# Performance work log

Measured on AMD Instinct MI355X. Metric: run time of the kernel, lower is better.

The kernel has to match this reference:

```python
import jax, jax.numpy as jnp
import numpy as np

STEP = 5
ALPHA = 0.01
D = 1024
BN_EPS = 1e-5
L2_EPS = 1e-12


def setup_inputs() -> dict:
    key = jax.random.key(0)
    k1, k2 = jax.random.split(key, 2)
    B = 16
    x = jax.random.normal(k1, (B * STEP, D), dtype=jnp.float32)
    W = jax.random.normal(k2, (D, D), dtype=jnp.float32) * 0.02
    b = jnp.zeros((D,), jnp.float32)
    gamma = jnp.ones((D,), jnp.float32)
    beta = jnp.zeros((D,), jnp.float32)
    return {"x": x, "W": W, "b": b, "gamma": gamma, "beta": beta}


def reference(x, W, b, gamma, beta):
    BS = x.shape[0]          # B * STEP
    B = BS // STEP
    x_seq = x.reshape(B, STEP, D)

    def step_fn(h, xt):
        # xt: [B, D]; Hebbian fast-weight update
        # hebb = alpha * (k v^T - k^2 * h)
        hebb = ALPHA * (xt[:, :, None] * xt[:, None, :] - (xt ** 2)[:, :, None] * h)
        h = h + hebb
        return h, h

    h0 = jnp.zeros((B, D, D), x.dtype)
    _, mems = jax.lax.scan(step_fn, h0, jnp.swapaxes(x_seq, 0, 1))  # [STEP, B, D, D]
    # torch.cat(memory_total, dim=0) -> step-major stacking
    mem = mems.reshape(BS, D, D)

    # batched mat-vec readout; x here is batch-major (faithful to original mismatch)
    q = jnp.einsum('nij,nj->ni', mem, x)  # [BS, D]

    y = q @ W.T + b
    # BatchNorm1d in training mode: batch statistics, biased variance
    mu = y.mean(axis=0)
    var = y.var(axis=0)
    yhat = (y - mu) / jnp.sqrt(var + BN_EPS)
    out = jax.nn.relu(yhat * gamma + beta)
    # F.normalize: L2 over dim=1 with eps clamp
    norm = jnp.linalg.norm(out, axis=1, keepdims=True)
    return out / jnp.maximum(norm, L2_EPS)
```

## Files before the change

kernel.cpp:

```cpp
#include <hip/hip_runtime.h>
#include <math.h>

#define D_DIM   1024
#define BS      80
#define STEPS   5
#define ALPHA   0.01f
#define BN_EPS  1e-5f
#define L2_EPS  1e-12f

#define K2_NN   10
#define NG      8
#define A_BLOCKS 512

__global__ __launch_bounds__(256, 2) void kA(const float* __restrict__ x,
                                             const float* __restrict__ W,
                                             const float* __restrict__ bvec,
                                             float* __restrict__ y,
                                             float* __restrict__ psum,
                                             float* __restrict__ psq) {
    const int tid  = threadIdx.x;
    const int lane = tid & 63;
    const int wid  = tid >> 6;
    const int bid  = blockIdx.x;
    const int wave = bid * 4 + wid;
    const int jg   = wave & 255;
    const int j0   = jg * 4;
    const int ng   = bid >> 6;
    const int n0   = ng * K2_NN;

    __shared__ float qs[K2_NN][D_DIM];

    const float4* __restrict__ x4 = (const float4*)x;
    const float4* __restrict__ W4 = (const float4*)W;

    float4 w[4][4];
#pragma unroll
    for (int jj = 0; jj < 4; ++jj)
#pragma unroll
        for (int m = 0; m < 4; ++m)
            w[jj][m] = W4[(size_t)(j0 + jj) * 256 + lane + 64 * m];
    const float4 b4 = ((const float4*)bvec)[jg];

    for (int r = wid; r < K2_NN; r += 4) {
        const int n  = n0 + r;
        const int t  = n >> 4;
        const int bb = n & 15;

        float4 v[4];
#pragma unroll
        for (int m = 0; m < 4; ++m)
            v[m] = x4[(size_t)n * 256 + lane + 64 * m];

        float4 k[STEPS][4];
        float p[STEPS];
#pragma unroll
        for (int s = 0; s < STEPS; ++s) {
            if (s <= t) {
#pragma unroll
                for (int m = 0; m < 4; ++m)
                    k[s][m] = x4[(size_t)(bb * STEPS + s) * 256 + lane + 64 * m];
                float d = 0.f;
#pragma unroll
                for (int m = 0; m < 4; ++m)
                    d += k[s][m].x * v[m].x + k[s][m].y * v[m].y
                       + k[s][m].z * v[m].z + k[s][m].w * v[m].w;
                p[s] = d;
            } else {
                p[s] = 0.f;
            }
        }
#pragma unroll
        for (int off = 32; off; off >>= 1) {
#pragma unroll
            for (int s = 0; s < STEPS; ++s) p[s] += __shfl_xor(p[s], off, 64);
        }

        float4 acc[4];
#pragma unroll
        for (int m = 0; m < 4; ++m) acc[m] = make_float4(0.f, 0.f, 0.f, 0.f);
#pragma unroll
        for (int s = 0; s < STEPS; ++s) {
            if (s <= t) {
#pragma unroll
                for (int m = 0; m < 4; ++m) {
                    acc[m].x = acc[m].x * (1.f - ALPHA * k[s][m].x * k[s][m].x) + p[s] * k[s][m].x;
                    acc[m].y = acc[m].y * (1.f - ALPHA * k[s][m].y * k[s][m].y) + p[s] * k[s][m].y;
                    acc[m].z = acc[m].z * (1.f - ALPHA * k[s][m].z * k[s][m].z) + p[s] * k[s][m].z;
                    acc[m].w = acc[m].w * (1.f - ALPHA * k[s][m].w * k[s][m].w) + p[s] * k[s][m].w;
                }
            }
        }
#pragma unroll
        for (int m = 0; m < 4; ++m) {
            acc[m].x *= ALPHA; acc[m].y *= ALPHA; acc[m].z *= ALPHA; acc[m].w *= ALPHA;
            ((float4*)qs[r])[lane + 64 * m] = acc[m];
        }
    }
    __syncthreads();

    float csum[4] = {0.f, 0.f, 0.f, 0.f};
    float csq [4] = {0.f, 0.f, 0.f, 0.f};

#pragma unroll 2
    for (int nn = 0; nn < K2_NN; ++nn) {
        const int n = n0 + nn;
        float4 qv[4];
#pragma unroll
        for (int m = 0; m < 4; ++m)
            qv[m] = ((const float4*)qs[nn])[lane + 64 * m];

        float s[4] = {0.f, 0.f, 0.f, 0.f};
#pragma unroll
        for (int jj = 0; jj < 4; ++jj) {
#pragma unroll
            for (int m = 0; m < 4; ++m) {
                s[jj] += w[jj][m].x * qv[m].x + w[jj][m].y * qv[m].y
                       + w[jj][m].z * qv[m].z + w[jj][m].w * qv[m].w;
            }
        }
#pragma unroll
        for (int off = 32; off; off >>= 1) {
#pragma unroll
            for (int jj = 0; jj < 4; ++jj) s[jj] += __shfl_xor(s[jj], off, 64);
        }
        if (lane == 0) {
            float4 yv = make_float4(s[0] + b4.x, s[1] + b4.y,
                                    s[2] + b4.z, s[3] + b4.w);
            ((float4*)y)[(size_t)n * 256 + jg] = yv;
            csum[0] += yv.x; csum[1] += yv.y; csum[2] += yv.z; csum[3] += yv.w;
            csq[0] += yv.x * yv.x; csq[1] += yv.y * yv.y;
            csq[2] += yv.z * yv.z; csq[3] += yv.w * yv.w;
        }
    }
    if (lane == 0) {
        ((float4*)psum)[ng * 256 + jg] = make_float4(csum[0], csum[1], csum[2], csum[3]);
        ((float4*)psq )[ng * 256 + jg] = make_float4(csq [0], csq [1], csq [2], csq [3]);
    }
}

__global__ __launch_bounds__(256) void kB(const float* __restrict__ y,
                                          const float* __restrict__ psum,
                                          const float* __restrict__ psq,
                                          const float* __restrict__ gamma,
                                          const float* __restrict__ beta,
                                          float* __restrict__ out) {
    const int n   = blockIdx.x;
    const int tid = threadIdx.x;

    float4 su = make_float4(0.f, 0.f, 0.f, 0.f);
    float4 sq = make_float4(0.f, 0.f, 0.f, 0.f);
#pragma unroll
    for (int g = 0; g < NG; ++g) {
        const float4 a = ((const float4*)psum)[g * 256 + tid];
        const float4 b = ((const float4*)psq )[g * 256 + tid];
        su.x += a.x; su.y += a.y; su.z += a.z; su.w += a.w;
        sq.x += b.x; sq.y += b.y; sq.z += b.z; sq.w += b.w;
    }
    const float inv_bs = 1.f / (float)BS;
    const float4 yv = ((const float4*)y)[(size_t)n * 256 + tid];
    const float4 g4 = ((const float4*)gamma)[tid];
    const float4 be = ((const float4*)beta)[tid];

    float4 o;
    {
        const float mu = su.x * inv_bs;
        const float istd = rsqrtf(sq.x * inv_bs - mu * mu + BN_EPS);
        o.x = fmaxf((yv.x - mu) * istd * g4.x + be.x, 0.f);
    }
    {
        const float mu = su.y * inv_bs;
        const float istd = rsqrtf(sq.y * inv_bs - mu * mu + BN_EPS);
        o.y = fmaxf((yv.y - mu) * istd * g4.y + be.y, 0.f);
    }
    {
        const float mu = su.z * inv_bs;
        const float istd = rsqrtf(sq.z * inv_bs - mu * mu + BN_EPS);
        o.z = fmaxf((yv.z - mu) * istd * g4.z + be.z, 0.f);
    }
    {
        const float mu = su.w * inv_bs;
        const float istd = rsqrtf(sq.w * inv_bs - mu * mu + BN_EPS);
        o.w = fmaxf((yv.w - mu) * istd * g4.w + be.w, 0.f);
    }

    float ss = o.x * o.x + o.y * o.y + o.z * o.z + o.w * o.w;
#pragma unroll
    for (int off = 32; off; off >>= 1) ss += __shfl_xor(ss, off, 64);
    __shared__ float sred[4];
    if ((tid & 63) == 0) sred[tid >> 6] = ss;
    __syncthreads();
    const float stot = sred[0] + sred[1] + sred[2] + sred[3];

    const float scale = 1.f / fmaxf(sqrtf(stot), L2_EPS);
    float4 ov = make_float4(o.x * scale, o.y * scale, o.z * scale, o.w * scale);
    ((float4*)out)[(size_t)n * 256 + tid] = ov;
}

extern "C" void kernel_launch(void* const* d_in, const int* in_sizes, int n_in,
                              void* d_out, int out_size, void* d_ws, size_t ws_size,
                              hipStream_t stream) {
    const float* x     = (const float*)d_in[0];
    const float* W     = (const float*)d_in[1];
    const float* bvec  = (const float*)d_in[2];
    const float* gamma = (const float*)d_in[3];
    const float* beta  = (const float*)d_in[4];

    float* y    = (float*)d_ws;
    float* psum = y + BS * D_DIM;
    float* psq  = psum + NG * D_DIM;

    float* out = (float*)d_out;

    kA<<<A_BLOCKS, 256, 0, stream>>>(x, W, bvec, y, psum, psq);
    kB<<<BS,       256, 0, stream>>>(y, psum, psq, gamma, beta, out);
}
```

Before: 81.27 us.

## Split fast-weight readout into a separate kernel to avoid redundant q recomputation

```diff
diff --git a/kernel.cpp b/kernel.cpp
--- a/kernel.cpp
+++ b/kernel.cpp
@@ -8,11 +8,63 @@
 #define BN_EPS  1e-5f
 #define L2_EPS  1e-12f
 
-#define K2_NN   10
 #define NG      8
-#define A_BLOCKS 512
-
-__global__ __launch_bounds__(256, 2) void kA(const float* __restrict__ x,
+#define NROWS   10
+#define JBLK    128
+#define G_BLOCKS (NG * JBLK)
+
+__global__ __launch_bounds__(256) void kQ(const float* __restrict__ x,
+                                          float* __restrict__ q) {
+    const int n    = blockIdx.x;
+    const int tid  = threadIdx.x;
+    const int lane = tid & 63;
+    const int wid  = tid >> 6;
+    const int t    = n >> 4;
+    const int bb   = n & 15;
+
+    const float4* __restrict__ xv = (const float4*)(x + (size_t)n * D_DIM);
+    const float4 v = xv[tid];
+
+    float4 k[STEPS];
+#pragma unroll
+    for (int s = 0; s < STEPS; ++s)
+        k[s] = ((const float4*)(x + (size_t)(bb * STEPS + s) * D_DIM))[tid];
+
+    float p[STEPS];
+#pragma unroll
+    for (int s = 0; s < STEPS; ++s)
+        p[s] = k[s].x * v.x + k[s].y * v.y + k[s].z * v.z + k[s].w * v.w;
+
+#pragma unroll
+    for (int off = 32; off; off >>= 1) {
+#pragma unroll
+        for (int s = 0; s < STEPS; ++s) p[s] += __shfl_xor(p[s], off, 64);
+    }
+
+    __shared__ float sh[4][STEPS];
+    if (lane == 0) {
+#pragma unroll
+        for (int s = 0; s < STEPS; ++s) sh[wid][s] = p[s];
+    }
+    __syncthreads();
+    float c[STEPS];
+#pragma unroll
+    for (int s = 0; s < STEPS; ++s)
+        c[s] = sh[0][s] + sh[1][s] + sh[2][s] + sh[3][s];
+
+    float4 acc = make_float4(0.f, 0.f, 0.f, 0.f);
+    for (int s = 0; s <= t; ++s) {
+        const float4 xs = k[s];
+        acc.x = acc.x * (1.f - ALPHA * xs.x * xs.x) + c[s] * xs.x;
+        acc.y = acc.y * (1.f - ALPHA * xs.y * xs.y) + c[s] * xs.y;
+        acc.z = acc.z * (1.f - ALPHA * xs.z * xs.z) + c[s] * xs.z;
+        acc.w = acc.w * (1.f - ALPHA * xs.w * xs.w) + c[s] * xs.w;
+    }
+    acc.x *= ALPHA; acc.y *= ALPHA; acc.z *= ALPHA; acc.w *= ALPHA;
+    ((float4*)(q + (size_t)n * D_DIM))[tid] = acc;
+}
+
+__global__ __launch_bounds__(256, 4) void kG(const float* __restrict__ q,
                                              const float* __restrict__ W,
                                              const float* __restrict__ bvec,
                                              float* __restrict__ y,
@@ -22,119 +74,68 @@
     const int lane = tid & 63;
     const int wid  = tid >> 6;
     const int bid  = blockIdx.x;
-    const int wave = bid * 4 + wid;
-    const int jg   = wave & 255;
-    const int j0   = jg * 4;
-    const int ng   = bid >> 6;
-    const int n0   = ng * K2_NN;
-
-    __shared__ float qs[K2_NN][D_DIM];
-
-    const float4* __restrict__ x4 = (const float4*)x;
+    const int ng   = bid >> 7;
+    const int jb   = bid & 127;
+    const int j0   = jb * 8;
+    const int n0   = ng * NROWS;
+    const int jw   = j0 + wid * 2;
+
+    __shared__ float qs[NROWS][D_DIM];
+
     const float4* __restrict__ W4 = (const float4*)W;
-
-    float4 w[4][4];
-#pragma unroll
-    for (int jj = 0; jj < 4; ++jj)
+    float4 w[2][4];
+#pragma unroll
+    for (int jj = 0; jj < 2; ++jj)
 #pragma unroll
         for (int m = 0; m < 4; ++m)
-            w[jj][m] = W4[(size_t)(j0 + jj) * 256 + lane + 64 * m];
-    const float4 b4 = ((const float4*)bvec)[jg];
-
-    for (int r = wid; r < K2_NN; r += 4) {
-        const int n  = n0 + r;
-        const int t  = n >> 4;
-        const int bb = n & 15;
-
-        float4 v[4];
-#pragma unroll
-        for (int m = 0; m < 4; ++m)
-            v[m] = x4[(size_t)n * 256 + lane + 64 * m];
-
-        float4 k[STEPS][4];
-        float p[STEPS];
-#pragma unroll
-        for (int s = 0; s < STEPS; ++s) {
-            if (s <= t) {
-#pragma unroll
-                for (int m = 0; m < 4; ++m)
-                    k[s][m] = x4[(size_t)(bb * STEPS + s) * 256 + lane + 64 * m];
-                float d = 0.f;
-#pragma unroll
-                for (int m = 0; m < 4; ++m)
-                    d += k[s][m].x * v[m].x + k[s][m].y * v[m].y
-                       + k[s][m].z * v[m].z + k[s][m].w * v[m].w;
-                p[s] = d;
-            } else {
-                p[s] = 0.f;
-            }
-        }
-#pragma unroll
-        for (int off = 32; off; off >>= 1) {
-#pragma unroll
-            for (int s = 0; s < STEPS; ++s) p[s] += __shfl_xor(p[s], off, 64);
-        }
-
-        float4 acc[4];
-#pragma unroll
-        for (int m = 0; m < 4; ++m) acc[m] = make_float4(0.f, 0.f, 0.f, 0.f);
-#pragma unroll
-        for (int s = 0; s < STEPS; ++s) {
-            if (s <= t) {
-#pragma unroll
-                for (int m = 0; m < 4; ++m) {
-                    acc[m].x = acc[m].x * (1.f - ALPHA * k[s][m].x * k[s][m].x) + p[s] * k[s][m].x;
-                    acc[m].y = acc[m].y * (1.f - ALPHA * k[s][m].y * k[s][m].y) + p[s] * k[s][m].y;
-                    acc[m].z = acc[m].z * (1.f - ALPHA * k[s][m].z * k[s][m].z) + p[s] * k[s][m].z;
-                    acc[m].w = acc[m].w * (1.f - ALPHA * k[s][m].w * k[s][m].w) + p[s] * k[s][m].w;
-                }
-            }
-        }
-#pragma unroll
-        for (int m = 0; m < 4; ++m) {
-            acc[m].x *= ALPHA; acc[m].y *= ALPHA; acc[m].z *= ALPHA; acc[m].w *= ALPHA;
-            ((float4*)qs[r])[lane + 64 * m] = acc[m];
-        }
+            w[jj][m] = W4[(size_t)(jw + jj) * 256 + lane + 64 * m];
+    const float b0 = bvec[jw];
+    const float b1 = bvec[jw + 1];
+
+    {
+        const float4* __restrict__ q4 = (const float4*)(q + (size_t)n0 * D_DIM);
+        float4* __restrict__ qs4 = (float4*)qs;
+#pragma unroll
+        for (int i = 0; i < (NROWS * 256) / 256; ++i)
+            qs4[tid + 256 * i] = q4[tid + 256 * i];
     }
     __syncthreads();
 
-    float csum[4] = {0.f, 0.f, 0.f, 0.f};
-    float csq [4] = {0.f, 0.f, 0.f, 0.f};
+    float csum[2] = {0.f, 0.f};
+    float csq [2] = {0.f, 0.f};
 
 #pragma unroll 2
-    for (int nn = 0; nn < K2_NN; ++nn) {
+    for (int nn = 0; nn < NROWS; ++nn) {
         const int n = n0 + nn;
         float4 qv[4];
 #pragma unroll
         for (int m = 0; m < 4; ++m)
             qv[m] = ((const float4*)qs[nn])[lane + 64 * m];
 
-        float s[4] = {0.f, 0.f, 0.f, 0.f};
-#pragma unroll
-        for (int jj = 0; jj < 4; ++jj) {
-#pragma unroll
-            for (int m = 0; m < 4; ++m) {
-                s[jj] += w[jj][m].x * qv[m].x + w[jj][m].y * qv[m].y
-                       + w[jj][m].z * qv[m].z + w[jj][m].w * qv[m].w;
-            }
+        float s0 = 0.f, s1 = 0.f;
+#pragma unroll
+        for (int m = 0; m < 4; ++m) {
+            s0 += w[0][m].x * qv[m].x + w[0][m].y * qv[m].y
+                + w[0][m].z * qv[m].z + w[0][m].w * qv[m].w;
+            s1 += w[1][m].x * qv[m].x + w[1][m].y * qv[m].y
+                + w[1][m].z * qv[m].z + w[1][m].w * qv[m].w;
         }
 #pragma unroll
         for (int off = 32; off; off >>= 1) {
-#pragma unroll
-            for (int jj = 0; jj < 4; ++jj) s[jj] += __shfl_xor(s[jj], off, 64);
+            s0 += __shfl_xor(s0, off, 64);
+            s1 += __shfl_xor(s1, off, 64);
         }
         if (lane == 0) {
-            float4 yv = make_float4(s[0] + b4.x, s[1] + b4.y,
-                                    s[2] + b4.z, s[3] + b4.w);
-            ((float4*)y)[(size_t)n * 256 + jg] = yv;
-            csum[0] += yv.x; csum[1] += yv.y; csum[2] += yv.z; csum[3] += yv.w;
-            csq[0] += yv.x * yv.x; csq[1] += yv.y * yv.y;
-            csq[2] += yv.z * yv.z; csq[3] += yv.w * yv.w;
+            const float y0 = s0 + b0;
+            const float y1 = s1 + b1;
+            ((float2*)(y + (size_t)n * D_DIM + jw))[0] = make_float2(y0, y1);
+            csum[0] += y0; csum[1] += y1;
+            csq [0] += y0 * y0; csq [1] += y1 * y1;
         }
     }
     if (lane == 0) {
-        ((float4*)psum)[ng * 256 + jg] = make_float4(csum[0], csum[1], csum[2], csum[3]);
-        ((float4*)psq )[ng * 256 + jg] = make_float4(csq [0], csq [1], csq [2], csq [3]);
+        ((float2*)(psum + (size_t)ng * D_DIM + jw))[0] = make_float2(csum[0], csum[1]);
+        ((float2*)(psq  + (size_t)ng * D_DIM + jw))[0] = make_float2(csq [0], csq [1]);
     }
 }
 
@@ -205,12 +206,14 @@
     const float* gamma = (const float*)d_in[3];
     const float* beta  = (const float*)d_in[4];
 
-    float* y    = (float*)d_ws;
+    float* q    = (float*)d_ws;
+    float* y    = q + BS * D_DIM;
     float* psum = y + BS * D_DIM;
     float* psq  = psum + NG * D_DIM;
 
     float* out = (float*)d_out;
 
-    kA<<<A_BLOCKS, 256, 0, stream>>>(x, W, bvec, y, psum, psq);
+    kQ<<<BS,       256, 0, stream>>>(x, q);
+    kG<<<G_BLOCKS, 256, 0, stream>>>(q, W, bvec, y, psum, psq);
     kB<<<BS,       256, 0, stream>>>(y, psum, psq, gamma, beta, out);
 }
```

Result: faster. 78.91 us (-2.9%).
